# Optimization experiments

Hardware: AMD Instinct MI355X
Metric: run time of the kernel (lower is better)

## Reference

```python
import jax, jax.numpy as jnp
import numpy as np

N = 8192          # batch of labeled text embeddings
D = 256           # embedding dim
NUM_LABELS = 128  # distinct cluster labels


def setup_inputs() -> dict:
    key = jax.random.key(0)
    k1, k2 = jax.random.split(key)
    embeddings = jax.random.normal(k1, (N, D), dtype=jnp.float32)
    labels = jax.random.randint(k2, (N,), 0, NUM_LABELS, dtype=jnp.int64)
    logit_scale = jnp.array([20.0], dtype=jnp.float32)  # 1 / temperature, temperature=0.05
    return {"embeddings": embeddings, "labels": labels, "logit_scale": logit_scale}


def reference(embeddings, labels, logit_scale):
    # Equivalent reformulation of the per-group python loop:
    # for each label group g with >=2 members,
    #   contribution = (sum_{j!=k in g} exp(-s*sim_jk)) * (sum_{j in g, l not in g} exp(s*sim_jl))
    # loss = log(1 + sum_g contribution)
    s = logit_scale[0]
    eps = 1e-12  # matches torch F.normalize clamp
    e = embeddings / jnp.maximum(jnp.linalg.norm(embeddings, axis=1, keepdims=True), eps)
    S = (e @ e.T) * s                                   # [N, N] scaled cosine similarity
    n = labels.shape[0]
    same = labels[:, None] == labels[None, :]           # [N, N] same-label mask
    offdiag = ~jnp.eye(n, dtype=bool)
    pos_mask = same & offdiag                           # same label, j != k
    neg_mask = ~same                                    # different label
    # per-row partial sums (fused exp+mask+reduce under jit)
    a = jnp.sum(jnp.exp(-S) * pos_mask, axis=1)         # [N] positive-pair terms
    b = jnp.sum(jnp.exp(S) * neg_mask, axis=1)          # [N] negative-pair terms
    # aggregate per label group
    counts = jax.ops.segment_sum(jnp.ones((n,), dtype=jnp.float32), labels, num_segments=NUM_LABELS)
    A = jax.ops.segment_sum(a, labels, num_segments=NUM_LABELS)
    B = jax.ops.segment_sum(b, labels, num_segments=NUM_LABELS)
    valid = counts >= 2.0                               # groups with <2 members are skipped
    sum_value = 1.0 + jnp.sum(jnp.where(valid, A * B, 0.0))
    return jnp.log(sum_value)
```

## Files before the change

kernel.cpp:

```cpp
#include <hip/hip_runtime.h>
#include <hip/hip_bf16.h>
#include <math.h>


typedef __attribute__((ext_vector_type(2))) long l2;
typedef __attribute__((ext_vector_type(4))) float f32x4;

#define N_EMB 8192
#define D_EMB 256
#define NUM_LABELS 128
#define PAN 128
#define NPAN (N_EMB / PAN)
#define NTRI (NPAN * (NPAN + 1) / 2)

template <int CTRL>
__device__ __forceinline__ float dpp_add(float x) {
    int y = __builtin_amdgcn_update_dpp(0, __builtin_bit_cast(int, x),
                                        CTRL, 0xF, 0xF, false);
    return x + __builtin_bit_cast(float, y);
}
__device__ __forceinline__ float red16(float x) {
    x = dpp_add<0xB1>(x);
    x = dpp_add<0x4E>(x);
    x = dpp_add<0x124>(x);
    x = dpp_add<0x128>(x);
    return x;
}

__device__ __forceinline__ unsigned packbf(float a, float b) {
    unsigned ua = __builtin_bit_cast(unsigned, a);
    unsigned ub = __builtin_bit_cast(unsigned, b);
    ua += 0x7FFFu + ((ua >> 16) & 1u);
    ub += 0x7FFFu + ((ub >> 16) & 1u);
    return (ua >> 16) | (ub & 0xFFFF0000u);
}

__global__ __launch_bounds__(256) void normalize_kernel(const float* __restrict__ emb,
                                                        char* __restrict__ e8) {
    const int wid = threadIdx.x >> 6, lane = threadIdx.x & 63;
    const int row = blockIdx.x * 4 + wid;
    const f32x4 x = *(const f32x4*)(emb + (size_t)row * D_EMB + lane * 4);
    float ss = x[0]*x[0] + x[1]*x[1] + x[2]*x[2] + x[3]*x[3];
    #pragma unroll
    for (int off = 32; off >= 1; off >>= 1) ss += __shfl_xor(ss, off);
    const float r = 1.0f / fmaxf(sqrtf(ss), 1e-12f);
    int v = __builtin_amdgcn_cvt_pk_fp8_f32(x[0] * r, x[1] * r, 0, false);
    v = __builtin_amdgcn_cvt_pk_fp8_f32(x[2] * r, x[3] * r, v, true);
    const int u    = lane >> 4;
    const int half = (lane >> 3) & 1;
    const int lp   = ((lane >> 1) & 3) * 16 + (row & 15);
    const int j0   = (lane & 1) * 4;
    char* dst = e8 + ((size_t)(row >> 4) * 4 + u) * 1024 + lp * 16 + half * 8 + j0;
    *(unsigned*)dst = (unsigned)v;
}

#define LOADF(dst, voff, sb, OFFSTR) \
    asm volatile("global_load_dwordx4 %0, %1, %2 offset:" OFFSTR \
                 : "=v"(dst) : "v"(voff), "s"(sb))

#define ISSUE(PA_, PB_, OFFSTR) \
    LOADF(PA_[0], voA[0], sbA, OFFSTR); LOADF(PA_[1], voA[1], sbA, OFFSTR); \
    LOADF(PA_[2], voA[2], sbA, OFFSTR); LOADF(PA_[3], voA[3], sbA, OFFSTR); \
    LOADF(PB_[0], voB[0], sbB, OFFSTR); LOADF(PB_[1], voB[1], sbB, OFFSTR); \
    LOADF(PB_[2], voB[2], sbB, OFFSTR); LOADF(PB_[3], voB[3], sbB, OFFSTR)

#define WAITV(NSTR) \
    asm volatile("s_waitcnt vmcnt(" NSTR ")" ::: "memory"); \
    __builtin_amdgcn_sched_barrier(0)

#define MF8(a, b, c) __builtin_amdgcn_mfma_f32_16x16x32_fp8_fp8(a, b, c, 0, 0, 0)

#define MROW(PA_, PB_, mi, H) \
    acc[mi][0] = MF8(PA_[mi][H], PB_[0][H], acc[mi][0]); \
    acc[mi][1] = MF8(PA_[mi][H], PB_[1][H], acc[mi][1]); \
    acc[mi][2] = MF8(PA_[mi][H], PB_[2][H], acc[mi][2]); \
    acc[mi][3] = MF8(PA_[mi][H], PB_[3][H], acc[mi][3]);

#define MFMA32(PA_, PB_) \
    __builtin_amdgcn_s_setprio(1); \
    MROW(PA_, PB_, 0, 0) MROW(PA_, PB_, 1, 0) MROW(PA_, PB_, 2, 0) MROW(PA_, PB_, 3, 0) \
    MROW(PA_, PB_, 0, 1) MROW(PA_, PB_, 1, 1) MROW(PA_, PB_, 2, 1) MROW(PA_, PB_, 3, 1) \
    __builtin_amdgcn_s_setprio(0)

__global__ __launch_bounds__(256, 3) void cosent_main(const char* __restrict__ e8,
                                                      const int* __restrict__ labels,
                                                      const float* __restrict__ scale,
                                                      unsigned* __restrict__ wsAB) {
    __shared__ float rowsc[2][PAN][2];
    __shared__ float colsc[2][PAN][2];
    __shared__ int labR[PAN], labC[PAN];

    const int bid = blockIdx.x;
    const int swz = (bid & 7) * 260 + (bid >> 3);
    int rem = swz, by = 0;
    while (rem >= NPAN - by) { rem -= NPAN - by; ++by; }
    const int bx = by + rem;
    const bool diag = (bx == by);
    const int rowBase = by * PAN, colBase = bx * PAN;

    const int tid = threadIdx.x, lane = tid & 63, wid = tid >> 6;
    const int wm = wid >> 1, wn = wid & 1;
    const int rr = lane & 15, kh = lane >> 4;

    if (tid < PAN) labR[tid] = labels[rowBase + tid];
    else           labC[tid - PAN] = labels[colBase + tid - PAN];
    __syncthreads();

    const int laneB = lane * 16;
    int voA[4], voB[4];
    #pragma unroll
    for (int i = 0; i < 4; ++i) {
        voA[i] = (wm * 4 + i) * 4096 + laneB;
        voB[i] = (wn * 4 + i) * 4096 + laneB;
    }
    const char* sbA = e8 + (size_t)rowBase * 256;
    const char* sbB = e8 + (size_t)colBase * 256;

    f32x4 acc[4][4];
    #pragma unroll
    for (int i = 0; i < 4; ++i)
        #pragma unroll
        for (int j = 0; j < 4; ++j) acc[i][j] = (f32x4){0.f, 0.f, 0.f, 0.f};

    l2 pA[4], pB[4], qA[4], qB[4];

    ISSUE(pA, pB, "0");
    ISSUE(qA, qB, "1024"); WAITV("8"); MFMA32(pA, pB);
    ISSUE(pA, pB, "2048"); WAITV("8"); MFMA32(qA, qB);
    ISSUE(qA, qB, "3072"); WAITV("8"); MFMA32(pA, pB);
    WAITV("0"); MFMA32(qA, qB);

    const float s = *scale;
    int lc[4];
    #pragma unroll
    for (int ni = 0; ni < 4; ++ni) lc[ni] = labC[wn * 64 + ni * 16 + rr];
    float colA[4] = {0.f, 0.f, 0.f, 0.f}, colB[4] = {0.f, 0.f, 0.f, 0.f};

    #pragma unroll
    for (int mi = 0; mi < 4; ++mi) {
        #pragma unroll
        for (int r = 0; r < 4; ++r) {
            const int rowL = wm * 64 + mi * 16 + kh * 4 + r;
            const int lr = labR[rowL];
            float asum = 0.f, bsum = 0.f;
            #pragma unroll
            for (int ni = 0; ni < 4; ++ni) {
                const int colL = wn * 64 + ni * 16 + rr;
                const float val = acc[mi][ni][r] * s;
                const bool pos = (lr == lc[ni]);
                float ex = __expf(pos ? -val : val);
                if (diag && rowL == colL) ex = 0.f;
                if (pos) { asum += ex; colA[ni] += ex; }
                else     { bsum += ex; colB[ni] += ex; }
            }
            asum = red16(asum);
            bsum = red16(bsum);
            if (rr == 0) { rowsc[wn][rowL][0] = asum; rowsc[wn][rowL][1] = bsum; }
        }
    }

    if (!diag) {
        #pragma unroll
        for (int ni = 0; ni < 4; ++ni) {
            float a = colA[ni], b = colB[ni];
            a += __shfl_xor(a, 16); a += __shfl_xor(a, 32);
            b += __shfl_xor(b, 16); b += __shfl_xor(b, 32);
            if (lane < 16) {
                colsc[wm][wn * 64 + ni * 16 + lane][0] = a;
                colsc[wm][wn * 64 + ni * 16 + lane][1] = b;
            }
        }
    }
    __syncthreads();

    if (tid < PAN) {
        const float ra = rowsc[0][tid][0] + rowsc[1][tid][0];
        const float rb = rowsc[0][tid][1] + rowsc[1][tid][1];
        wsAB[(size_t)bx * N_EMB + rowBase + tid] = packbf(ra, rb);
        if (!diag) {
            const float ca = colsc[0][tid][0] + colsc[1][tid][0];
            const float cb = colsc[0][tid][1] + colsc[1][tid][1];
            wsAB[(size_t)by * N_EMB + colBase + tid] = packbf(ca, cb);
        }
    }
}

__global__ __launch_bounds__(256) void reduce_rows(const unsigned* __restrict__ wsAB,
                                                   const int* __restrict__ labels,
                                                   float* __restrict__ part) {
    __shared__ float A[NUM_LABELS], B[NUM_LABELS];
    __shared__ int C[NUM_LABELS];
    const int tid = threadIdx.x;
    if (tid < NUM_LABELS) { A[tid] = 0.f; B[tid] = 0.f; C[tid] = 0; }
    __syncthreads();
    const int row = blockIdx.x * 256 + tid;
    float a = 0.f, b = 0.f;
    #pragma unroll
    for (int p = 0; p < NPAN; ++p) {
        const unsigned u = wsAB[(size_t)p * N_EMB + row];
        a += __builtin_bit_cast(float, u << 16);
        b += __builtin_bit_cast(float, u & 0xFFFF0000u);
    }
    const int l = labels[row];
    atomicAdd(&A[l], a);
    atomicAdd(&B[l], b);
    atomicAdd(&C[l], 1);
    __syncthreads();
    if (tid < NUM_LABELS) {
        float* p = part + ((size_t)blockIdx.x * NUM_LABELS + tid) * 3;
        p[0] = A[tid]; p[1] = B[tid]; p[2] = (float)C[tid];
    }
}

__global__ __launch_bounds__(128) void finalize_kernel(const float* __restrict__ part,
                                                       float* __restrict__ out) {
    const int tid = threadIdx.x;
    float A = 0.f, B = 0.f, c = 0.f;
    #pragma unroll
    for (int blk = 0; blk < 32; ++blk) {
        const float* p = part + ((size_t)blk * NUM_LABELS + tid) * 3;
        A += p[0]; B += p[1]; c += p[2];
    }
    float v = (c >= 2.f) ? A * B : 0.f;
    #pragma unroll
    for (int off = 32; off >= 1; off >>= 1) v += __shfl_xor(v, off);
    __shared__ float w2[2];
    if ((tid & 63) == 0) w2[tid >> 6] = v;
    __syncthreads();
    if (tid == 0) out[0] = logf(1.0f + w2[0] + w2[1]);
}

extern "C" void kernel_launch(void* const* d_in, const int* in_sizes, int n_in,
                              void* d_out, int out_size, void* d_ws, size_t ws_size,
                              hipStream_t stream) {
    const float* emb    = (const float*)d_in[0];
    const int*   labels = (const int*)d_in[1];
    const float* scale  = (const float*)d_in[2];
    float* out = (float*)d_out;

    char*     e8   = (char*)d_ws;
    unsigned* wsAB = (unsigned*)((char*)d_ws + (size_t)N_EMB * D_EMB);
    float*    part = (float*)((char*)wsAB + (size_t)NPAN * N_EMB * sizeof(unsigned));

    normalize_kernel<<<N_EMB / 4, 256, 0, stream>>>(emb, e8);
    cosent_main<<<NTRI, 256, 0, stream>>>(e8, labels, scale, wsAB);
    reduce_rows<<<N_EMB / 256, 256, 0, stream>>>(wsAB, labels, part);
    finalize_kernel<<<1, 128, 0, stream>>>(part, out);
}
```

Measured before the change: 47.14 us.

## Fold scale into fp8 embeddings, use hw exp2, closed-form tile index, wider reduce

The normalize kernel now multiplies each row by sqrt(scale*log2 e), so the MFMA output is already the log2-scaled logit and the epilogue can call v_exp_f32 directly. This drops a multiply and the exp scaling per element. The triangular tile index is computed with a sqrt formula plus correction loops instead of a linear loop, and the label __syncthreads is moved after the MFMA loads. The row reduction is spread over 128 blocks with 4 waves each, and finalize reads the larger partial buffer. Pre-scaling before fp8 quantization changes the value range, which may alter precision (e4m3 max ~448; scaled values up to ~5.4).

```diff
diff --git a/kernel.cpp b/kernel.cpp
--- a/kernel.cpp
+++ b/kernel.cpp
@@ -27,6 +27,12 @@
     return x;
 }
 
+__device__ __forceinline__ float exp2hw(float x) {
+    float r;
+    asm("v_exp_f32 %0, %1" : "=v"(r) : "v"(x));
+    return r;
+}
+
 __device__ __forceinline__ unsigned packbf(float a, float b) {
     unsigned ua = __builtin_bit_cast(unsigned, a);
     unsigned ub = __builtin_bit_cast(unsigned, b);
@@ -36,6 +42,7 @@
 }
 
 __global__ __launch_bounds__(256) void normalize_kernel(const float* __restrict__ emb,
+                                                        const float* __restrict__ scale,
                                                         char* __restrict__ e8) {
     const int wid = threadIdx.x >> 6, lane = threadIdx.x & 63;
     const int row = blockIdx.x * 4 + wid;
@@ -44,8 +51,9 @@
     #pragma unroll
     for (int off = 32; off >= 1; off >>= 1) ss += __shfl_xor(ss, off);
     const float r = 1.0f / fmaxf(sqrtf(ss), 1e-12f);
-    int v = __builtin_amdgcn_cvt_pk_fp8_f32(x[0] * r, x[1] * r, 0, false);
-    v = __builtin_amdgcn_cvt_pk_fp8_f32(x[2] * r, x[3] * r, v, true);
+    const float ps = sqrtf(scale[0] * 1.44269504088896f) * r;
+    int v = __builtin_amdgcn_cvt_pk_fp8_f32(x[0] * ps, x[1] * ps, 0, false);
+    v = __builtin_amdgcn_cvt_pk_fp8_f32(x[2] * ps, x[3] * ps, v, true);
     const int u    = lane >> 4;
     const int half = (lane >> 3) & 1;
     const int lp   = ((lane >> 1) & 3) * 16 + (row & 15);
@@ -84,7 +92,6 @@
 
 __global__ __launch_bounds__(256, 3) void cosent_main(const char* __restrict__ e8,
                                                       const int* __restrict__ labels,
-                                                      const float* __restrict__ scale,
                                                       unsigned* __restrict__ wsAB) {
     __shared__ float rowsc[2][PAN][2];
     __shared__ float colsc[2][PAN][2];
@@ -92,9 +99,11 @@
 
     const int bid = blockIdx.x;
     const int swz = (bid & 7) * 260 + (bid >> 3);
-    int rem = swz, by = 0;
-    while (rem >= NPAN - by) { rem -= NPAN - by; ++by; }
-    const int bx = by + rem;
+    int by = (int)((129.0f - sqrtf(16641.0f - 8.0f * (float)swz)) * 0.5f);
+    by = by < 0 ? 0 : (by > 63 ? 63 : by);
+    while (by < 63 && (by + 1) * (129 - (by + 1)) / 2 <= swz) ++by;
+    while (by > 0 && by * (129 - by) / 2 > swz) --by;
+    const int bx = by + (swz - by * (129 - by) / 2);
     const bool diag = (bx == by);
     const int rowBase = by * PAN, colBase = bx * PAN;
 
@@ -104,7 +113,6 @@
 
     if (tid < PAN) labR[tid] = labels[rowBase + tid];
     else           labC[tid - PAN] = labels[colBase + tid - PAN];
-    __syncthreads();
 
     const int laneB = lane * 16;
     int voA[4], voB[4];
@@ -130,7 +138,8 @@
     ISSUE(qA, qB, "3072"); WAITV("8"); MFMA32(pA, pB);
     WAITV("0"); MFMA32(qA, qB);
 
-    const float s = *scale;
+    __syncthreads();
+
     int lc[4];
     #pragma unroll
     for (int ni = 0; ni < 4; ++ni) lc[ni] = labC[wn * 64 + ni * 16 + rr];
@@ -146,9 +155,9 @@
             #pragma unroll
             for (int ni = 0; ni < 4; ++ni) {
                 const int colL = wn * 64 + ni * 16 + rr;
-                const float val = acc[mi][ni][r] * s;
+                const float val = acc[mi][ni][r];
                 const bool pos = (lr == lc[ni]);
-                float ex = __expf(pos ? -val : val);
+                float ex = exp2hw(pos ? -val : val);
                 if (diag && rowL == colL) ex = 0.f;
                 if (pos) { asum += ex; colA[ni] += ex; }
                 else     { bsum += ex; colB[ni] += ex; }
@@ -188,46 +197,52 @@
 __global__ __launch_bounds__(256) void reduce_rows(const unsigned* __restrict__ wsAB,
                                                    const int* __restrict__ labels,
                                                    float* __restrict__ part) {
-    __shared__ float A[NUM_LABELS], B[NUM_LABELS];
-    __shared__ int C[NUM_LABELS];
-    const int tid = threadIdx.x;
-    if (tid < NUM_LABELS) { A[tid] = 0.f; B[tid] = 0.f; C[tid] = 0; }
-    __syncthreads();
-    const int row = blockIdx.x * 256 + tid;
+    __shared__ float sA[4][64], sB[4][64];
+    __shared__ float binA[NUM_LABELS], binB[NUM_LABELS];
+    __shared__ int binC[NUM_LABELS];
+    const int tid = threadIdx.x, lane = tid & 63, wid = tid >> 6;
+    if (tid < NUM_LABELS) { binA[tid] = 0.f; binB[tid] = 0.f; binC[tid] = 0; }
+    const int rowBase = blockIdx.x * 64;
     float a = 0.f, b = 0.f;
     #pragma unroll
-    for (int p = 0; p < NPAN; ++p) {
-        const unsigned u = wsAB[(size_t)p * N_EMB + row];
+    for (int p = 0; p < 16; ++p) {
+        const unsigned u = wsAB[(size_t)(wid * 16 + p) * N_EMB + rowBase + lane];
         a += __builtin_bit_cast(float, u << 16);
         b += __builtin_bit_cast(float, u & 0xFFFF0000u);
     }
-    const int l = labels[row];
-    atomicAdd(&A[l], a);
-    atomicAdd(&B[l], b);
-    atomicAdd(&C[l], 1);
+    sA[wid][lane] = a; sB[wid][lane] = b;
+    __syncthreads();
+    if (tid < 64) {
+        const float A = sA[0][tid] + sA[1][tid] + sA[2][tid] + sA[3][tid];
+        const float B = sB[0][tid] + sB[1][tid] + sB[2][tid] + sB[3][tid];
+        const int l = labels[rowBase + tid];
+        atomicAdd(&binA[l], A);
+        atomicAdd(&binB[l], B);
+        atomicAdd(&binC[l], 1);
+    }
     __syncthreads();
     if (tid < NUM_LABELS) {
         float* p = part + ((size_t)blockIdx.x * NUM_LABELS + tid) * 3;
-        p[0] = A[tid]; p[1] = B[tid]; p[2] = (float)C[tid];
+        p[0] = binA[tid]; p[1] = binB[tid]; p[2] = (float)binC[tid];
     }
 }
 
 __global__ __launch_bounds__(128) void finalize_kernel(const float* __restrict__ part,
                                                        float* __restrict__ out) {
-    const int tid = threadIdx.x;
+    const int g = threadIdx.x;
     float A = 0.f, B = 0.f, c = 0.f;
-    #pragma unroll
-    for (int blk = 0; blk < 32; ++blk) {
-        const float* p = part + ((size_t)blk * NUM_LABELS + tid) * 3;
+    #pragma unroll 8
+    for (int b = 0; b < 128; ++b) {
+        const float* p = part + ((size_t)b * NUM_LABELS + g) * 3;
         A += p[0]; B += p[1]; c += p[2];
     }
     float v = (c >= 2.f) ? A * B : 0.f;
     #pragma unroll
     for (int off = 32; off >= 1; off >>= 1) v += __shfl_xor(v, off);
     __shared__ float w2[2];
-    if ((tid & 63) == 0) w2[tid >> 6] = v;
-    __syncthreads();
-    if (tid == 0) out[0] = logf(1.0f + w2[0] + w2[1]);
+    if ((g & 63) == 0) w2[g >> 6] = v;
+    __syncthreads();
+    if (g == 0) out[0] = logf(1.0f + w2[0] + w2[1]);
 }
 
 extern "C" void kernel_launch(void* const* d_in, const int* in_sizes, int n_in,
@@ -238,12 +253,13 @@
     const float* scale  = (const float*)d_in[2];
     float* out = (float*)d_out;
 
-    char*     e8   = (char*)d_ws;
-    unsigned* wsAB = (unsigned*)((char*)d_ws + (size_t)N_EMB * D_EMB);
-    float*    part = (float*)((char*)wsAB + (size_t)NPAN * N_EMB * sizeof(unsigned));
-
-    normalize_kernel<<<N_EMB / 4, 256, 0, stream>>>(emb, e8);
-    cosent_main<<<NTRI, 256, 0, stream>>>(e8, labels, scale, wsAB);
-    reduce_rows<<<N_EMB / 256, 256, 0, stream>>>(wsAB, labels, part);
+    char* base = (char*)d_ws;
+    char*     e8   = base;
+    unsigned* wsAB = (unsigned*)(base + (2u << 20));
+    float*    part = (float*)(base + (4u << 20));
+
+    normalize_kernel<<<N_EMB / 4, 256, 0, stream>>>(emb, scale, e8);
+    cosent_main<<<NTRI, 256, 0, stream>>>(e8, labels, wsAB);
+    reduce_rows<<<NUM_LABELS, 256, 0, stream>>>(wsAB, labels, part);
     finalize_kernel<<<1, 128, 0, stream>>>(part, out);
 }
```

Measured after the change: 47.80 us. Within noise of the previous version (+1.4%).
